# Optimization experiments

Measured on AMD Instinct MI355X. Metric: run time of the kernel, lower is better.

Reference implementation:

```python
import jax, jax.numpy as jnp
import numpy as np

# ---- config derived from init_kwargs (level=3, max_levels=14, max_size=256,
# max_channels=512, margin=10, start_cutoff=2, critical_layers=2, window_size=6) ----
SCALE_FACTOR = 2          # size_prev(16) < size(32)
UP_FACTOR = 2 * SCALE_FACTOR   # 4
UP_PAD = (13, 10)         # p = 24 - 2*sf = 20 -> ((p+1)//2 + 2*sf - 1, p//2)
DOWN_PAD = (5, 5)         # p = 12 - 2 = 10 -> ((p+1)//2, p//2)
MARGIN = 10
CUTOFF, BAND_HALF = 5.656854249492381, 10.343145750507619   # level 3, sr=128
CUTOFF_PREV, BAND_HALF_PREV = 4.0, 4.0                      # level 2, sr=128
SR = 32 * SCALE_FACTOR * 2  # 128


def _lowpass_filter(n_taps, cutoff, band_half, sr):
    # Kaiser-windowed sinc lowpass, identical math to the torch module.
    df = 2 * band_half / (sr / 2)
    atten = 2.285 * (n_taps - 1) * np.pi * df + 7.95
    if atten > 50:
        beta = 0.1102 * (atten - 8.7)
    elif atten >= 21:
        beta = 0.5842 * (atten - 21) ** 0.4 + 0.07886 * (atten - 21)
    else:
        beta = 0.0
    ind = np.arange(n_taps) - (n_taps - 1) / 2
    window = np.i0(beta * np.sqrt(1 - (2 * ind / (n_taps - 1)) ** 2)) / np.i0(beta)
    return 2 * cutoff / sr * np.sinc(2 * cutoff / sr * ind) * window


def setup_inputs() -> dict:
    key = jax.random.key(0)
    x = jax.random.normal(key, (16, 512, 36, 36), dtype=jnp.float32)
    up = _lowpass_filter(24, CUTOFF_PREV, BAND_HALF_PREV, SR)
    up = up / up.sum() * 2 * SCALE_FACTOR
    down = _lowpass_filter(12, CUTOFF, BAND_HALF, SR)
    down = down / down.sum()
    return {
        "x": x,
        "up_filter": jnp.asarray(up, dtype=jnp.float32),
        "down_filter": jnp.asarray(down, dtype=jnp.float32),
    }


def _upfirdn1d(x, kernel, up, down, pad, axis):
    # Separable 1D upfirdn along axis (2=H, 3=W) of NCHW tensor.
    # Matches upfirdn2d_native: zero-insert upsample (up-1 trailing zeros),
    # pad, correlate with flipped kernel, stride-`down` decimate.
    # lhs_dilation inserts up-1 zeros BETWEEN samples; adding up-1 to the
    # right pad reproduces the trailing zeros of the native op exactly.
    B, C, H, W = x.shape
    k = kernel.shape[0]
    w = jnp.flip(kernel).astype(x.dtype)
    if axis == 3:
        rhs = w.reshape(1, 1, 1, k)
        lhs_dil, strides = (1, up), (1, down)
        padding = ((0, 0), (pad[0], pad[1] + up - 1))
    else:
        rhs = w.reshape(1, 1, k, 1)
        lhs_dil, strides = (up, 1), (down, 1)
        padding = ((pad[0], pad[1] + up - 1), (0, 0))
    y = jax.lax.conv_general_dilated(
        x.reshape(B * C, 1, H, W), rhs,
        window_strides=strides, padding=padding, lhs_dilation=lhs_dil,
        dimension_numbers=("NCHW", "OIHW", "NCHW"))
    return y.reshape(B, C, y.shape[2], y.shape[3])


def reference(x, up_filter, down_filter):
    # Upsample x4 (separable: width then height)
    x = _upfirdn1d(x, up_filter, UP_FACTOR, 1, UP_PAD, axis=3)
    x = _upfirdn1d(x, up_filter, UP_FACTOR, 1, UP_PAD, axis=2)   # (16,512,144,144)
    # Pointwise nonlinearity in the high-res domain (alias-free)
    x = jax.nn.leaky_relu(x, 0.2)
    # Downsample x2 (separable: width then height)
    x = _upfirdn1d(x, down_filter, 1, 2, DOWN_PAD, axis=3)
    x = _upfirdn1d(x, down_filter, 1, 2, DOWN_PAD, axis=2)       # (16,512,72,72)
    m = SCALE_FACTOR * MARGIN // 2  # 10
    return x[:, :, m:-m, m:-m]      # (16,512,52,52)
```

## Files before the change

### kernel.cpp

```cpp
#include <hip/hip_runtime.h>


__global__ __launch_bounds__(256, 4)
void afa_kernel(const float* __restrict__ x,
                const float* __restrict__ upf,
                const float* __restrict__ dnf,
                float* __restrict__ out)
{
    __shared__ float tH[114 * 35];
    __shared__ float t2[114 * 53];

    const int plane = blockIdx.x;
    const int tid   = threadIdx.x;
    const float* __restrict__ xp = x + (size_t)plane * (36 * 36);
    float* __restrict__ op       = out + (size_t)plane * (52 * 52);

    float up[24];
#pragma unroll
    for (int i = 0; i < 24; ++i) up[i] = upf[i];

    if (tid < 204) {
        const int s  = tid / 34;
        const int mw = tid % 34 + 1;

        float xr[11];
#pragma unroll
        for (int jj = 0; jj < 11; ++jj) {
            int row = 5 * s + 1 + jj;
            row = row > 35 ? 35 : row;
            xr[jj] = xp[row * 36 + mw];
        }
        const int lh0  = 20 * s;
        const int jmax = (s == 5) ? 14 : 20;
#pragma unroll
        for (int j = 0; j < 20; ++j) {
            if (j < jmax) {
                const int rel = ((j + 5) >> 2) - 1;
                const int c0  = 20 + ((j + 1) & 3);
                float acc = 0.f;
#pragma unroll
                for (int t = 0; t < 6; ++t)
                    acc = fmaf(xr[rel + t], up[c0 - 4 * t], acc);
                tH[(lh0 + j) * 35 + (mw - 1)] = acc;
            }
        }
    }
    __syncthreads();

    float dn[12];
#pragma unroll
    for (int i = 0; i < 12; ++i) dn[i] = dnf[i];

    if (tid < 228) {
        const int lh = tid % 114;
        const int p  = tid / 114;

        float r[21];
#pragma unroll
        for (int jj = 0; jj < 21; ++jj)
            r[jj] = tH[lh * 35 + 13 * p + jj];

        float acc[26];
#pragma unroll
        for (int o = 0; o < 26; ++o) acc[o] = 0.f;

#pragma unroll
        for (int j = 0; j < 62; ++j) {
            const int rel = ((j + 5) >> 2) - 1;
            const int c0  = 20 + ((j + 1) & 3);
            float h = 0.f;
#pragma unroll
            for (int t = 0; t < 6; ++t)
                h = fmaf(r[rel + t], up[c0 - 4 * t], h);
            h = h < 0.f ? 0.2f * h : h;
#pragma unroll
            for (int k = 0; k < 12; ++k) {
                const int jk = j - k;
                if (jk >= 0 && (jk & 1) == 0 && (jk >> 1) < 26) {
                    acc[jk >> 1] = fmaf(h, dn[11 - k], acc[jk >> 1]);
                }
            }
        }
#pragma unroll
        for (int o = 0; o < 26; ++o)
            t2[lh * 53 + 26 * p + o] = acc[o];
    }
    __syncthreads();

    if (tid < 208) {
        const int ow = tid % 52;
        const int s  = tid / 52;

        float rr[36];
#pragma unroll
        for (int jj = 0; jj < 36; ++jj)
            rr[jj] = t2[(26 * s + jj) * 53 + ow];

#pragma unroll
        for (int j = 0; j < 13; ++j) {
            float acc = 0.f;
#pragma unroll
            for (int k = 0; k < 12; ++k)
                acc = fmaf(rr[2 * j + k], dn[11 - k], acc);
            op[(13 * s + j) * 52 + ow] = acc;
        }
    }
}

extern "C" void kernel_launch(void* const* d_in, const int* in_sizes, int n_in,
                              void* d_out, int out_size, void* d_ws, size_t ws_size,
                              hipStream_t stream)
{
    const float* x  = (const float*)d_in[0];
    const float* up = (const float*)d_in[1];
    const float* dn = (const float*)d_in[2];
    float* out = (float*)d_out;

    const int planes = 16 * 512;
    afa_kernel<<<dim3(planes), dim3(256), 0, stream>>>(x, up, dn, out);
}
```

Before: 149.9 us.

## Process two planes per block with packed float2 FMA math

Each block now handles two channel planes at once, keeping them as 2-wide float vectors so the compiler can emit packed FP32 FMAs (v_pk_fma_f32 on CDNA). The two shared buffers are merged into one v2f buffer, with an extra barrier so the first stage's region can be reused by the second stage's output. The leaky ReLU becomes min/max/fma so it stays vectorised. In exchange, register use and LDS per block roughly double, occupancy is lowered to 3 blocks per CU, and only half as many blocks are launched.

```diff
diff --git a/kernel.cpp b/kernel.cpp
--- a/kernel.cpp
+++ b/kernel.cpp
@@ -1,34 +1,43 @@
 #include <hip/hip_runtime.h>
 
 
-__global__ __launch_bounds__(256, 4)
+typedef float v2f __attribute__((ext_vector_type(2)));
+
+static __device__ __forceinline__ v2f vsplat(float s) { v2f v; v.x = s; v.y = s; return v; }
+
+__global__ __launch_bounds__(256, 3)
 void afa_kernel(const float* __restrict__ x,
                 const float* __restrict__ upf,
                 const float* __restrict__ dnf,
                 float* __restrict__ out)
 {
-    __shared__ float tH[114 * 35];
-    __shared__ float t2[114 * 53];
+    __shared__ v2f buf[114 * 53];
 
-    const int plane = blockIdx.x;
-    const int tid   = threadIdx.x;
-    const float* __restrict__ xp = x + (size_t)plane * (36 * 36);
-    float* __restrict__ op       = out + (size_t)plane * (52 * 52);
+    const int tid = threadIdx.x;
+    const size_t q0 = (size_t)blockIdx.x * 2;
+    const float* __restrict__ xp0 = x + q0 * (36 * 36);
+    const float* __restrict__ xp1 = xp0 + (36 * 36);
+    float* __restrict__ op0 = out + q0 * (52 * 52);
+    float* __restrict__ op1 = op0 + (52 * 52);
 
     float up[24];
 #pragma unroll
     for (int i = 0; i < 24; ++i) up[i] = upf[i];
+    float dn[12];
+#pragma unroll
+    for (int i = 0; i < 12; ++i) dn[i] = dnf[i];
 
     if (tid < 204) {
         const int s  = tid / 34;
         const int mw = tid % 34 + 1;
 
-        float xr[11];
+        v2f xr[11];
 #pragma unroll
         for (int jj = 0; jj < 11; ++jj) {
             int row = 5 * s + 1 + jj;
             row = row > 35 ? 35 : row;
-            xr[jj] = xp[row * 36 + mw];
+            xr[jj].x = xp0[row * 36 + mw];
+            xr[jj].y = xp1[row * 36 + mw];
         }
         const int lh0  = 20 * s;
         const int jmax = (s == 5) ? 14 : 20;
@@ -37,53 +46,52 @@
             if (j < jmax) {
                 const int rel = ((j + 5) >> 2) - 1;
                 const int c0  = 20 + ((j + 1) & 3);
-                float acc = 0.f;
+                v2f acc = vsplat(0.f);
 #pragma unroll
                 for (int t = 0; t < 6; ++t)
-                    acc = fmaf(xr[rel + t], up[c0 - 4 * t], acc);
-                tH[(lh0 + j) * 35 + (mw - 1)] = acc;
+                    acc = __builtin_elementwise_fma(xr[rel + t], vsplat(up[c0 - 4 * t]), acc);
+                buf[(lh0 + j) * 35 + (mw - 1)] = acc;
             }
         }
     }
     __syncthreads();
 
-    float dn[12];
+    const int lh = tid % 114;
+    const int p  = tid / 114;
+    v2f r[21];
+    if (tid < 228) {
 #pragma unroll
-    for (int i = 0; i < 12; ++i) dn[i] = dnf[i];
+        for (int jj = 0; jj < 21; ++jj)
+            r[jj] = buf[lh * 35 + 13 * p + jj];
+    }
+    __syncthreads();
 
     if (tid < 228) {
-        const int lh = tid % 114;
-        const int p  = tid / 114;
-
-        float r[21];
+        v2f acc[26];
 #pragma unroll
-        for (int jj = 0; jj < 21; ++jj)
-            r[jj] = tH[lh * 35 + 13 * p + jj];
-
-        float acc[26];
-#pragma unroll
-        for (int o = 0; o < 26; ++o) acc[o] = 0.f;
+        for (int o = 0; o < 26; ++o) acc[o] = vsplat(0.f);
 
 #pragma unroll
         for (int j = 0; j < 62; ++j) {
             const int rel = ((j + 5) >> 2) - 1;
             const int c0  = 20 + ((j + 1) & 3);
-            float h = 0.f;
+            v2f h = vsplat(0.f);
 #pragma unroll
             for (int t = 0; t < 6; ++t)
-                h = fmaf(r[rel + t], up[c0 - 4 * t], h);
-            h = h < 0.f ? 0.2f * h : h;
+                h = __builtin_elementwise_fma(r[rel + t], vsplat(up[c0 - 4 * t]), h);
+            v2f hneg = __builtin_elementwise_min(h, vsplat(0.f));
+            v2f hpos = __builtin_elementwise_max(h, vsplat(0.f));
+            h = __builtin_elementwise_fma(hneg, vsplat(0.2f), hpos);
 #pragma unroll
             for (int k = 0; k < 12; ++k) {
                 const int jk = j - k;
-                if (jk >= 0 && (jk & 1) == 0 && (jk >> 1) < 26) {
-                    acc[jk >> 1] = fmaf(h, dn[11 - k], acc[jk >> 1]);
-                }
+                if (jk >= 0 && (jk & 1) == 0 && (jk >> 1) < 26)
+                    acc[jk >> 1] = __builtin_elementwise_fma(h, vsplat(dn[11 - k]), acc[jk >> 1]);
             }
         }
 #pragma unroll
         for (int o = 0; o < 26; ++o)
-            t2[lh * 53 + 26 * p + o] = acc[o];
+            buf[lh * 53 + 26 * p + o] = acc[o];
     }
     __syncthreads();
 
@@ -91,18 +99,20 @@
         const int ow = tid % 52;
         const int s  = tid / 52;
 
-        float rr[36];
+        v2f rr[36];
 #pragma unroll
         for (int jj = 0; jj < 36; ++jj)
-            rr[jj] = t2[(26 * s + jj) * 53 + ow];
+            rr[jj] = buf[(26 * s + jj) * 53 + ow];
 
 #pragma unroll
         for (int j = 0; j < 13; ++j) {
-            float acc = 0.f;
+            v2f acc = vsplat(0.f);
 #pragma unroll
             for (int k = 0; k < 12; ++k)
-                acc = fmaf(rr[2 * j + k], dn[11 - k], acc);
-            op[(13 * s + j) * 52 + ow] = acc;
+                acc = __builtin_elementwise_fma(rr[2 * j + k], vsplat(dn[11 - k]), acc);
+            const int o = (13 * s + j) * 52 + ow;
+            op0[o] = acc.x;
+            op1[o] = acc.y;
         }
     }
 }
@@ -116,6 +126,6 @@
     const float* dn = (const float*)d_in[2];
     float* out = (float*)d_out;
 
-    const int planes = 16 * 512;
-    afa_kernel<<<dim3(planes), dim3(256), 0, stream>>>(x, up, dn, out);
+    const int pairs = 16 * 512 / 2;
+    afa_kernel<<<dim3(pairs), dim3(256), 0, stream>>>(x, up, dn, out);
 }
```

After: 145.7 us. -2.8%, faster.
